# Kernel optimization log

Hardware: AMD Instinct MI355X
Metric: run time of the kernel (lower is better)

## Reference

```python
import jax, jax.numpy as jnp
import numpy as np

B, S, D, H = 2, 4096, 1024, 16
HD = D // H  # 64


def setup_inputs() -> dict:
    key = jax.random.key(0)
    ks = jax.random.split(key, 9)
    init = lambda k, shape: (jax.random.normal(k, shape, dtype=jnp.float32) * 0.02)
    return {
        "x": jax.random.normal(ks[0], (B, S, D), dtype=jnp.float32),
        "Wq": init(ks[1], (D, D)), "bq": init(ks[2], (D,)),
        "Wk": init(ks[3], (D, D)), "bk": init(ks[4], (D,)),
        "Wv": init(ks[5], (D, D)), "bv": init(ks[6], (D,)),
        "Wo": init(ks[7], (D, D)), "bo": init(ks[8], (D,)),
    }


def _split_heads(t):
    # [B, S, D] -> [B, H, S, HD]
    b, s, d = t.shape
    return t.reshape(b, s, H, HD).transpose(0, 2, 1, 3)


def reference(x, Wq, bq, Wk, bk, Wv, bv, Wo, bo):
    # q/k/v projections (torch Linear: x @ W.T + b)
    q = _split_heads(x @ Wq.T + bq)
    k = _split_heads(x @ Wk.T + bk)
    v = _split_heads(x @ Wv.T + bv)
    scale = 1.0 / np.sqrt(HD).astype(np.float32)
    # chunked_attention uses full K/V per chunk => equivalent to full attention.
    scores = jnp.einsum("bhqd,bhkd->bhqk", q, k) * scale
    # softmax computed in fp32 then cast back (matches F.softmax(dtype=float32))
    attn = jax.nn.softmax(scores.astype(jnp.float32), axis=-1).astype(scores.dtype)
    out = jnp.einsum("bhqk,bhkd->bhqd", attn, v)
    out = out.transpose(0, 2, 1, 3).reshape(B, S, D)  # combine heads
    return out @ Wo.T + bo
```

## Files before the change

### kernel.cpp

```cpp
#include <hip/hip_runtime.h>
#include <hip/hip_bf16.h>
#include <stdint.h>

typedef __attribute__((ext_vector_type(8))) short short8;
typedef __attribute__((ext_vector_type(4))) short short4v;
typedef __attribute__((ext_vector_type(4))) float f32x4;
typedef __attribute__((ext_vector_type(4))) unsigned int uint4v;

#define MFMA16(A, B, C) __builtin_amdgcn_mfma_f32_16x16x32_bf16(A, B, C, 0, 0, 0)

#define GLDS16(gp, lp) __builtin_amdgcn_global_load_lds(                     \
    (const __attribute__((address_space(1))) unsigned int*)(gp),             \
    (__attribute__((address_space(3))) unsigned int*)(lp), 16, 0, 0)

static constexpr int kS  = 4096;
static constexpr int kD  = 1024;
static constexpr int kH  = 16;
static constexpr int kHD = 64;

__device__ __forceinline__ short bf16_bits(float f) {
    __hip_bfloat16 h = __float2bfloat16(f);
    return *(short*)&h;
}

__device__ __forceinline__ unsigned int pk_bf16(float a, float b) {
    __hip_bfloat162 h = __float22bfloat162_rn(make_float2(a, b));
    return *(unsigned int*)&h;
}

__device__ __forceinline__ short8 cvt8(const float* __restrict__ p) {
    f32x4 a = ((const f32x4*)p)[0];
    f32x4 b = ((const f32x4*)p)[1];
    short8 r;
    r[0] = bf16_bits(a[0]); r[1] = bf16_bits(a[1]);
    r[2] = bf16_bits(a[2]); r[3] = bf16_bits(a[3]);
    r[4] = bf16_bits(b[0]); r[5] = bf16_bits(b[1]);
    r[6] = bf16_bits(b[2]); r[7] = bf16_bits(b[3]);
    return r;
}

__device__ __forceinline__ unsigned char f32_to_e4m3(float f) {
    unsigned int u = __float_as_uint(f);
    unsigned int s = (u >> 24) & 0x80u;
    unsigned int a = u & 0x7fffffffu;
    if (a < 0x3c800000u) {
        float af = __uint_as_float(a);
        unsigned int sub = (unsigned int)(af * 512.0f + 0.5f);
        return (unsigned char)(s | sub);
    }
    unsigned int r = a + 0x80000u;
    unsigned int m = (r >> 20) & 7u;
    int eb = (int)(r >> 23) - 127 + 7;
    unsigned int bits = ((unsigned int)eb << 3) | m;
    if (bits > 0x7Eu) bits = 0x7Eu;
    return (unsigned char)(s | bits);
}
__device__ __forceinline__ float e4m3_to_f32(unsigned int b) {
    unsigned int s = b & 0x80u;
    unsigned int e = (b >> 3) & 15u;
    unsigned int m = b & 7u;
    float f = e ? __uint_as_float(((e + 120u) << 23) | (m << 20))
                : (float)m * 0.001953125f;
    return s ? -f : f;
}

__global__ __launch_bounds__(256) void cvt_f32_bf16(
    const float* __restrict__ src, __hip_bfloat16* __restrict__ dst)
{
    const int i = blockIdx.x * 256 + threadIdx.x;
    f32x4 v = ((const f32x4*)src)[i];
    short4v o;
    o[0] = bf16_bits(v[0]); o[1] = bf16_bits(v[1]);
    o[2] = bf16_bits(v[2]); o[3] = bf16_bits(v[3]);
    ((short4v*)dst)[i] = o;
}

__global__ __launch_bounds__(256) void cvt_w4(
    const float* __restrict__ w0, const float* __restrict__ w1,
    const float* __restrict__ w2, const float* __restrict__ w3,
    __hip_bfloat16* __restrict__ dst)
{
    const int blk = blockIdx.x;
    const int sel = blk >> 10;
    const float* src = sel == 0 ? w0 : sel == 1 ? w1 : sel == 2 ? w2 : w3;
    const int i = (blk & 1023) * 256 + threadIdx.x;
    f32x4 v = ((const f32x4*)src)[i];
    short4v o;
    o[0] = bf16_bits(v[0]); o[1] = bf16_bits(v[1]);
    o[2] = bf16_bits(v[2]); o[3] = bf16_bits(v[3]);
    ((short4v*)(dst + (size_t)sel * kD * kD))[i] = o;
}


__global__ __launch_bounds__(256) void gemm_qkv(
    const __hip_bfloat16* __restrict__ X, const __hip_bfloat16* __restrict__ Wb,
    const float* __restrict__ bq, const float* __restrict__ bk,
    const float* __restrict__ bv,
    __hip_bfloat16* __restrict__ Qw, __hip_bfloat16* __restrict__ Kw,
    __hip_bfloat16* __restrict__ Vtw)
{
    __shared__ short As[128 * 64];
    __shared__ short Bs[128 * 64];

    const int lane = threadIdx.x & 63, wave = threadIdx.x >> 6;
    const int quad = lane >> 4, l16 = lane & 15;
    const int sel = blockIdx.y >> 3;
    const int m0 = blockIdx.x * 128, n0 = (blockIdx.y & 7) * 128;
    const int wm = wave & 1, wn = wave >> 1;

    const float* bias = sel == 0 ? bq : sel == 1 ? bk : bv;
    const short* Xg = (const short*)X + (size_t)m0 * kD;
    const short* Wg = (const short*)Wb + (size_t)sel * kD * kD + (size_t)n0 * kD;

    f32x4 acc[4][4];
    #pragma unroll
    for (int mt = 0; mt < 4; ++mt)
        #pragma unroll
        for (int nt = 0; nt < 4; ++nt) acc[mt][nt] = f32x4{0.f, 0.f, 0.f, 0.f};

    const int srow = lane >> 3;
    const int gch  = (lane & 7) ^ srow;

    for (int k0 = 0; k0 < kD; k0 += 64) {
        __syncthreads();
        #pragma unroll
        for (int i = 0; i < 4; ++i) {
            const int rowbase = wave * 32 + i * 8;
            const int row = rowbase + srow;
            GLDS16(Xg + (size_t)row * kD + k0 + gch * 8, &As[rowbase * 64]);
            GLDS16(Wg + (size_t)row * kD + k0 + gch * 8, &Bs[rowbase * 64]);
        }
        __syncthreads();

        #pragma unroll
        for (int c = 0; c < 2; ++c) {
            short8 af[4], bf[4];
            const int rx = l16 & 7;
            #pragma unroll
            for (int mt = 0; mt < 4; ++mt)
                af[mt] = *(const short8*)&As[(wm * 64 + mt * 16 + l16) * 64
                                             + (((c * 4 + quad) ^ rx) * 8)];
            #pragma unroll
            for (int nt = 0; nt < 4; ++nt)
                bf[nt] = *(const short8*)&Bs[(wn * 64 + nt * 16 + l16) * 64
                                             + (((c * 4 + quad) ^ rx) * 8)];
            #pragma unroll
            for (int mt = 0; mt < 4; ++mt)
                #pragma unroll
                for (int nt = 0; nt < 4; ++nt)
                    acc[mt][nt] = MFMA16(af[mt], bf[nt], acc[mt][nt]);
        }
    }

    #pragma unroll
    for (int nt = 0; nt < 4; ++nt) {
        const int n = n0 + wn * 64 + nt * 16 + l16;
        const float bvv = bias[n];
        #pragma unroll
        for (int mt = 0; mt < 4; ++mt) {
            if (sel == 2) {
                const int m = m0 + wm * 64 + mt * 16 + quad * 4;
                short4v pk;
                #pragma unroll
                for (int r = 0; r < 4; ++r)
                    pk[r] = bf16_bits(acc[mt][nt][r] + bvv);
                const int bh2 = (m >> 12) * kH + (n >> 6);
                short* dst = (short*)Vtw
                    + ((size_t)bh2 * kHD + (size_t)(n & (kHD - 1))) * kS
                    + (size_t)(m & (kS - 1));
                *(short4v*)dst = pk;
            } else {
                __hip_bfloat16* dst = sel == 0 ? Qw : Kw;
                const float scale = sel == 0 ? 0.18033688f : 1.0f;
                #pragma unroll
                for (int r = 0; r < 4; ++r) {
                    const int m = m0 + wm * 64 + mt * 16 + quad * 4 + r;
                    const float v = (acc[mt][nt][r] + bvv) * scale;
                    const size_t addr = (((size_t)(m >> 12) * kH + (n >> 6)) * kS
                                         + (size_t)(m & (kS - 1))) * kHD
                                        + (size_t)(n & (kHD - 1));
                    dst[addr] = __float2bfloat16(v);
                }
            }
        }
    }
}

__global__ __launch_bounds__(256) void gemm_out(
    const __hip_bfloat16* __restrict__ X, const __hip_bfloat16* __restrict__ W,
    const float* __restrict__ bias, float* __restrict__ out)
{
    __shared__ short As[128 * 64];
    __shared__ short Bs[128 * 64];

    const int lane = threadIdx.x & 63, wave = threadIdx.x >> 6;
    const int quad = lane >> 4, l16 = lane & 15;
    const int m0 = blockIdx.x * 128, n0 = blockIdx.y * 128;
    const int wm = wave & 1, wn = wave >> 1;

    const short* Xg = (const short*)X + (size_t)m0 * kD;
    const short* Wg = (const short*)W + (size_t)n0 * kD;

    f32x4 acc[4][4];
    #pragma unroll
    for (int mt = 0; mt < 4; ++mt)
        #pragma unroll
        for (int nt = 0; nt < 4; ++nt) acc[mt][nt] = f32x4{0.f, 0.f, 0.f, 0.f};

    const int srow = lane >> 3;
    const int gch  = (lane & 7) ^ srow;

    for (int k0 = 0; k0 < kD; k0 += 64) {
        __syncthreads();
        #pragma unroll
        for (int i = 0; i < 4; ++i) {
            const int rowbase = wave * 32 + i * 8;
            const int row = rowbase + srow;
            GLDS16(Xg + (size_t)row * kD + k0 + gch * 8, &As[rowbase * 64]);
            GLDS16(Wg + (size_t)row * kD + k0 + gch * 8, &Bs[rowbase * 64]);
        }
        __syncthreads();

        #pragma unroll
        for (int c = 0; c < 2; ++c) {
            short8 af[4], bf[4];
            const int rx = l16 & 7;
            #pragma unroll
            for (int mt = 0; mt < 4; ++mt)
                af[mt] = *(const short8*)&As[(wm * 64 + mt * 16 + l16) * 64
                                             + (((c * 4 + quad) ^ rx) * 8)];
            #pragma unroll
            for (int nt = 0; nt < 4; ++nt)
                bf[nt] = *(const short8*)&Bs[(wn * 64 + nt * 16 + l16) * 64
                                             + (((c * 4 + quad) ^ rx) * 8)];
            #pragma unroll
            for (int mt = 0; mt < 4; ++mt)
                #pragma unroll
                for (int nt = 0; nt < 4; ++nt)
                    acc[mt][nt] = MFMA16(af[mt], bf[nt], acc[mt][nt]);
        }
    }

    #pragma unroll
    for (int nt = 0; nt < 4; ++nt) {
        const int n = n0 + wn * 64 + nt * 16 + l16;
        const float bv = bias[n];
        #pragma unroll
        for (int mt = 0; mt < 4; ++mt)
            #pragma unroll
            for (int r = 0; r < 4; ++r) {
                const int m = m0 + wm * 64 + mt * 16 + quad * 4 + r;
                out[(size_t)m * kD + n] = acc[mt][nt][r] + bv;
            }
    }
}

__global__ __launch_bounds__(256, 4) void flash2(
    const __hip_bfloat16* __restrict__ Qw, const __hip_bfloat16* __restrict__ Kw,
    const __hip_bfloat16* __restrict__ Vt, __hip_bfloat16* __restrict__ O)
{
    __shared__ short Ks[2][8 * 512];
    __shared__ short Vs[2][8 * 512];

    const int lane = threadIdx.x & 63, wave = threadIdx.x >> 6;
    const int quad = lane >> 4, l16 = lane & 15;

    const int flat = blockIdx.y * 32 + blockIdx.x;
    const int swz  = (flat & 7) * 128 + (flat >> 3);
    const int bh = swz >> 5, b = bh >> 4, h = bh & 15;
    const int qbase = (swz & 31) * 128 + wave * 32;

    const short* Qg = (const short*)Qw + ((size_t)bh * kS + qbase) * kHD;
    short8 qf[2][2];
    #pragma unroll
    for (int t = 0; t < 2; ++t)
        #pragma unroll
        for (int c = 0; c < 2; ++c)
            qf[t][c] = *(const short8*)(Qg + (t * 16 + l16) * kHD + c * 32 + quad * 8);

    const short* Kg = (const short*)Kw + (size_t)bh * kS * kHD;
    const short* Vg = (const short*)Vt + (size_t)bh * kHD * kS;

    const short ONE = 0x3F80;
    const short8 onesf = {ONE, ONE, ONE, ONE, ONE, ONE, ONE, ONE};

    f32x4 o[2][4], lsumv[2];
    #pragma unroll
    for (int t = 0; t < 2; ++t) {
        lsumv[t] = f32x4{0.f, 0.f, 0.f, 0.f};
        #pragma unroll
        for (int dt = 0; dt < 4; ++dt) o[t][dt] = f32x4{0.f, 0.f, 0.f, 0.f};
    }

    const int kc = wave >> 1, km = wave & 1;
    const int krow = kc * 32 + 8 * (l16 >> 2) + 4 * km + (l16 & 3);
    const short* ka0 = Kg + (size_t)krow * kHD + quad * 8;
    const short* ka1 = ka0 + 32;
    const int vdt = (wave & 1) * 2, vc32 = (wave >> 1) * 32;
    const short* va0 = Vg + (size_t)((vdt + 0) * 16 + l16) * kS + vc32 + quad * 8;
    const short* va1 = Vg + (size_t)((vdt + 1) * 16 + l16) * kS + vc32 + quad * 8;

    GLDS16(ka0, &Ks[0][(wave * 2 + 0) * 512]);
    GLDS16(ka1, &Ks[0][(wave * 2 + 1) * 512]);
    GLDS16(va0, &Vs[0][(wave * 2 + 0) * 512]);
    GLDS16(va1, &Vs[0][(wave * 2 + 1) * 512]);
    ka0 += 64 * kHD; ka1 += 64 * kHD; va0 += 64; va1 += 64;

    for (int k0 = 0; k0 < kS; k0 += 64) {
        const int cur = (k0 >> 6) & 1;
        __syncthreads();
        if (k0 + 64 < kS) {
            const int nxt = cur ^ 1;
            GLDS16(ka0, &Ks[nxt][(wave * 2 + 0) * 512]);
            GLDS16(ka1, &Ks[nxt][(wave * 2 + 1) * 512]);
            GLDS16(va0, &Vs[nxt][(wave * 2 + 0) * 512]);
            GLDS16(va1, &Vs[nxt][(wave * 2 + 1) * 512]);
            ka0 += 64 * kHD; ka1 += 64 * kHD; va0 += 64; va1 += 64;
        }

        #pragma unroll
        for (int c = 0; c < 2; ++c) {
            short8 vb[4];
            #pragma unroll
            for (int dt = 0; dt < 4; ++dt)
                vb[dt] = *(const short8*)&Vs[cur][(c * 4 + dt) * 512 + lane * 8];

            unsigned int P[2][4];
            #pragma unroll
            for (int m = 0; m < 2; ++m) {
                const int fb = c * 4 + m * 2;
                short8 a0 = *(const short8*)&Ks[cur][(fb + 0) * 512 + lane * 8];
                short8 a1 = *(const short8*)&Ks[cur][(fb + 1) * 512 + lane * 8];
                #pragma unroll
                for (int t = 0; t < 2; ++t) {
                    f32x4 z = {0.f, 0.f, 0.f, 0.f};
                    f32x4 s = MFMA16(a0, qf[t][0], z);
                    s = MFMA16(a1, qf[t][1], s);
                    P[t][m * 2 + 0] = pk_bf16(__builtin_amdgcn_exp2f(s[0]),
                                              __builtin_amdgcn_exp2f(s[1]));
                    P[t][m * 2 + 1] = pk_bf16(__builtin_amdgcn_exp2f(s[2]),
                                              __builtin_amdgcn_exp2f(s[3]));
                }
            }

            short8 pa[2];
            #pragma unroll
            for (int t = 0; t < 2; ++t) {
                uint4v u = {P[t][0], P[t][1], P[t][2], P[t][3]};
                pa[t] = __builtin_bit_cast(short8, u);
            }

            __builtin_amdgcn_s_setprio(1);
            #pragma unroll
            for (int t = 0; t < 2; ++t)
                lsumv[t] = MFMA16(pa[t], onesf, lsumv[t]);
            #pragma unroll
            for (int dt = 0; dt < 4; ++dt) {
                o[0][dt] = MFMA16(pa[0], vb[dt], o[0][dt]);
                o[1][dt] = MFMA16(pa[1], vb[dt], o[1][dt]);
            }
            __builtin_amdgcn_s_setprio(0);
        }
    }

    #pragma unroll
    for (int t = 0; t < 2; ++t)
        #pragma unroll
        for (int r = 0; r < 4; ++r) {
            const float inv = 1.0f / lsumv[t][r];
            const int sq = qbase + t * 16 + quad * 4 + r;
            #pragma unroll
            for (int dt = 0; dt < 4; ++dt)
                O[((size_t)b * kS + sq) * kD + h * kHD + dt * 16 + l16] =
                    __float2bfloat16(o[t][dt][r] * inv);
        }
}

template <bool KV8, bool WB16>
__global__ __launch_bounds__(256) void gemm_kv(
    const float* __restrict__ X, const void* __restrict__ W,
    const float* __restrict__ bias, void* __restrict__ outv)
{
    const int lane = threadIdx.x & 63;
    const int wave = threadIdx.x >> 6;
    const int quad = lane >> 4;
    const int l16  = lane & 15;
    const int m0 = blockIdx.x * 16;
    const int n0 = blockIdx.y * 256 + wave * 64;

    const float* xr = X + (size_t)(m0 + l16) * kD;
    const float* wf = (const float*)W + (size_t)(n0 + l16) * kD;
    const short* wb = (const short*)W + (size_t)(n0 + l16) * kD;

    f32x4 acc[4] = {{0.f,0.f,0.f,0.f},{0.f,0.f,0.f,0.f},
                    {0.f,0.f,0.f,0.f},{0.f,0.f,0.f,0.f}};

    for (int k8 = quad; k8 < kD / 8; k8 += 4) {
        short8 a = cvt8(xr + k8 * 8);
        #pragma unroll
        for (int nt = 0; nt < 4; ++nt) {
            short8 w = WB16 ? *(const short8*)(wb + nt * 16 * kD + k8 * 8)
                            : cvt8(wf + nt * 16 * kD + k8 * 8);
            acc[nt] = MFMA16(a, w, acc[nt]);
        }
    }

    #pragma unroll
    for (int nt = 0; nt < 4; ++nt) {
        const int n = n0 + nt * 16 + l16;
        const float bv = bias[n];
        #pragma unroll
        for (int r = 0; r < 4; ++r) {
            const int m = m0 + quad * 4 + r;
            const float v = acc[nt][r] + bv;
            const size_t addr = (((size_t)(m >> 12) * kH + (n >> 6)) * kS
                                 + (size_t)(m & (kS - 1))) * kHD + (size_t)(n & (kHD - 1));
            if (KV8) ((unsigned char*)outv)[addr] = f32_to_e4m3(v);
            else     ((__hip_bfloat16*)outv)[addr] = __float2bfloat16(v);
        }
    }
}

template <bool KV8, bool WB16>
__global__ __launch_bounds__(256) void flash_fusedq(
    const float* __restrict__ x,  const void* __restrict__ Wq,
    const float* __restrict__ bq, const void* __restrict__ Kw,
    const void* __restrict__ Vw,  __hip_bfloat16* __restrict__ O)
{
    __shared__ short pool[9216];
    __shared__ short Ps[4][32][72];

    const int lane = threadIdx.x & 63;
    const int wave = threadIdx.x >> 6;
    const int quad = lane >> 4;
    const int l16  = lane & 15;
    const int bh   = blockIdx.y;
    const int b    = bh >> 4, h = bh & 15;
    const int qbase = blockIdx.x * 128 + wave * 32;

    {
        const float* xr0 = x + (size_t)(b * kS + qbase + l16) * kD;
        const float* xr1 = xr0 + (size_t)16 * kD;
        const float* wqf = (const float*)Wq + (size_t)(h * kHD + l16) * kD;
        const short* wqb = (const short*)Wq + (size_t)(h * kHD + l16) * kD;
        f32x4 qa[2][4];
        #pragma unroll
        for (int t = 0; t < 2; ++t)
            #pragma unroll
            for (int nt = 0; nt < 4; ++nt) qa[t][nt] = f32x4{0.f,0.f,0.f,0.f};

        for (int k8 = quad; k8 < kD / 8; k8 += 4) {
            short8 a0 = cvt8(xr0 + k8 * 8);
            short8 a1 = cvt8(xr1 + k8 * 8);
            #pragma unroll
            for (int nt = 0; nt < 4; ++nt) {
                short8 w = WB16 ? *(const short8*)(wqb + nt * 16 * kD + k8 * 8)
                                : cvt8(wqf + nt * 16 * kD + k8 * 8);
                qa[0][nt] = MFMA16(a0, w, qa[0][nt]);
                qa[1][nt] = MFMA16(a1, w, qa[1][nt]);
            }
        }
        #pragma unroll
        for (int t = 0; t < 2; ++t)
            #pragma unroll
            for (int nt = 0; nt < 4; ++nt) {
                const float bv = bq[h * kHD + nt * 16 + l16];
                #pragma unroll
                for (int r = 0; r < 4; ++r)
                    pool[wave * 2304 + (t * 16 + quad * 4 + r) * 72 + nt * 16 + l16] =
                        bf16_bits((qa[t][nt][r] + bv) * 0.125f);
            }
    }
    short8 qf[2][2];
    #pragma unroll
    for (int t = 0; t < 2; ++t)
        #pragma unroll
        for (int c = 0; c < 2; ++c)
            qf[t][c] = *(const short8*)&pool[wave * 2304 + (t * 16 + l16) * 72 + c * 32 + quad * 8];

    f32x4 o[2][4];
    float mrow[2][4], lrow[2][4];
    #pragma unroll
    for (int t = 0; t < 2; ++t)
        #pragma unroll
        for (int dt = 0; dt < 4; ++dt) o[t][dt] = f32x4{0.f,0.f,0.f,0.f};
    #pragma unroll
    for (int t = 0; t < 2; ++t)
        #pragma unroll
        for (int r = 0; r < 4; ++r) { mrow[t][r] = -INFINITY; lrow[t][r] = 0.f; }

    const __hip_bfloat16* Kb16 = (const __hip_bfloat16*)Kw + (size_t)bh * kS * kHD;
    const __hip_bfloat16* Vb16 = (const __hip_bfloat16*)Vw + (size_t)bh * kS * kHD;
    const unsigned char*  K8   = (const unsigned char*)Kw + (size_t)bh * kS * kHD;
    const unsigned char*  V8   = (const unsigned char*)Vw + (size_t)bh * kS * kHD;

    for (int k0 = 0; k0 < kS; k0 += 64) {
        __syncthreads();
        #pragma unroll
        for (int i = 0; i < 2; ++i) {
            const int lin = threadIdx.x + i * 256;
            const int kr = lin >> 3, c8 = lin & 7;
            short8 kv, vv;
            if (KV8) {
                uint2 kbits = *(const uint2*)(K8 + (size_t)(k0 + kr) * kHD + c8 * 8);
                uint2 vbits = *(const uint2*)(V8 + (size_t)(k0 + kr) * kHD + c8 * 8);
                #pragma unroll
                for (int j = 0; j < 4; ++j) {
                    kv[j]     = bf16_bits(e4m3_to_f32((kbits.x >> (8 * j)) & 255u));
                    kv[4 + j] = bf16_bits(e4m3_to_f32((kbits.y >> (8 * j)) & 255u));
                    vv[j]     = bf16_bits(e4m3_to_f32((vbits.x >> (8 * j)) & 255u));
                    vv[4 + j] = bf16_bits(e4m3_to_f32((vbits.y >> (8 * j)) & 255u));
                }
            } else {
                kv = *(const short8*)(Kb16 + (size_t)(k0 + kr) * kHD + c8 * 8);
                vv = *(const short8*)(Vb16 + (size_t)(k0 + kr) * kHD + c8 * 8);
            }
            *(short8*)&pool[kr * 72 + c8 * 8] = kv;
            #pragma unroll
            for (int j = 0; j < 8; ++j)
                pool[4608 + (c8 * 8 + j) * 72 + (((kr >> 3) ^ c8) << 3) + (kr & 7)] = vv[j];
        }
        __syncthreads();

        f32x4 sc[2][4];
        #pragma unroll
        for (int kt = 0; kt < 4; ++kt) {
            short8 b0 = *(const short8*)&pool[(kt * 16 + l16) * 72 + quad * 8];
            short8 b1 = *(const short8*)&pool[(kt * 16 + l16) * 72 + 32 + quad * 8];
            f32x4 z = {0.f, 0.f, 0.f, 0.f};
            f32x4 s0 = MFMA16(qf[0][0], b0, z); s0 = MFMA16(qf[0][1], b1, s0);
            f32x4 s1 = MFMA16(qf[1][0], b0, z); s1 = MFMA16(qf[1][1], b1, s1);
            sc[0][kt] = s0; sc[1][kt] = s1;
        }

        #pragma unroll
        for (int t = 0; t < 2; ++t)
            #pragma unroll
            for (int r = 0; r < 4; ++r) {
                float s0 = sc[t][0][r], s1 = sc[t][1][r];
                float s2 = sc[t][2][r], s3 = sc[t][3][r];
                float mx = fmaxf(fmaxf(s0, s1), fmaxf(s2, s3));
                #pragma unroll
                for (int off = 1; off < 16; off <<= 1)
                    mx = fmaxf(mx, __shfl_xor(mx, off, 64));
                const float mnew  = fmaxf(mrow[t][r], mx);
                const float alpha = __builtin_amdgcn_exp2f((mrow[t][r] - mnew) * 1.44269504f);
                mrow[t][r] = mnew;
                const float p0 = __builtin_amdgcn_exp2f((s0 - mnew) * 1.44269504f);
                const float p1 = __builtin_amdgcn_exp2f((s1 - mnew) * 1.44269504f);
                const float p2 = __builtin_amdgcn_exp2f((s2 - mnew) * 1.44269504f);
                const float p3 = __builtin_amdgcn_exp2f((s3 - mnew) * 1.44269504f);
                float ps = (p0 + p1) + (p2 + p3);
                #pragma unroll
                for (int off = 1; off < 16; off <<= 1)
                    ps += __shfl_xor(ps, off, 64);
                lrow[t][r] = lrow[t][r] * alpha + ps;
                o[t][0][r] *= alpha; o[t][1][r] *= alpha;
                o[t][2][r] *= alpha; o[t][3][r] *= alpha;
                const int row = t * 16 + quad * 4 + r;
                Ps[wave][row][l16]      = bf16_bits(p0);
                Ps[wave][row][16 + l16] = bf16_bits(p1);
                Ps[wave][row][32 + l16] = bf16_bits(p2);
                Ps[wave][row][48 + l16] = bf16_bits(p3);
            }

        short8 pa[2][2];
        #pragma unroll
        for (int t = 0; t < 2; ++t)
            #pragma unroll
            for (int c = 0; c < 2; ++c)
                pa[t][c] = *(const short8*)&Ps[wave][t * 16 + l16][c * 32 + quad * 8];
        #pragma unroll
        for (int c = 0; c < 2; ++c)
            #pragma unroll
            for (int dt = 0; dt < 4; ++dt) {
                const int d = dt * 16 + l16;
                short8 vb = *(const short8*)&pool[4608 + d * 72 + ((((c * 4 + quad)) ^ (d >> 3)) << 3)];
                o[0][dt] = MFMA16(pa[0][c], vb, o[0][dt]);
                o[1][dt] = MFMA16(pa[1][c], vb, o[1][dt]);
            }
    }

    #pragma unroll
    for (int t = 0; t < 2; ++t)
        #pragma unroll
        for (int r = 0; r < 4; ++r) {
            const float inv = 1.0f / lrow[t][r];
            const int sq = qbase + t * 16 + quad * 4 + r;
            #pragma unroll
            for (int dt = 0; dt < 4; ++dt)
                O[((size_t)b * kS + sq) * kD + h * kHD + dt * 16 + l16] =
                    __float2bfloat16(o[t][dt][r] * inv);
        }
}

template <bool WB16>
__global__ __launch_bounds__(256) void proj_out(
    const __hip_bfloat16* __restrict__ Xb, const void* __restrict__ W,
    const float* __restrict__ bias, float* __restrict__ out)
{
    const int lane = threadIdx.x & 63;
    const int wave = threadIdx.x >> 6;
    const int quad = lane >> 4;
    const int l16  = lane & 15;
    const int m0 = blockIdx.x * 16;
    const int n0 = blockIdx.y * 256 + wave * 64;

    const short8* xr = (const short8*)((const short*)Xb + (size_t)(m0 + l16) * kD);
    const float*  wf = (const float*)W + (size_t)(n0 + l16) * kD;
    const short*  wb = (const short*)W + (size_t)(n0 + l16) * kD;

    f32x4 acc[4] = {{0.f,0.f,0.f,0.f},{0.f,0.f,0.f,0.f},
                    {0.f,0.f,0.f,0.f},{0.f,0.f,0.f,0.f}};

    for (int k8 = quad; k8 < kD / 8; k8 += 4) {
        short8 a = xr[k8];
        #pragma unroll
        for (int nt = 0; nt < 4; ++nt) {
            short8 w = WB16 ? *(const short8*)(wb + nt * 16 * kD + k8 * 8)
                            : cvt8(wf + nt * 16 * kD + k8 * 8);
            acc[nt] = MFMA16(a, w, acc[nt]);
        }
    }

    #pragma unroll
    for (int nt = 0; nt < 4; ++nt) {
        const int n = n0 + nt * 16 + l16;
        const float bv = bias[n];
        #pragma unroll
        for (int r = 0; r < 4; ++r) {
            const int m = m0 + quad * 4 + r;
            out[(size_t)m * kD + n] = acc[nt][r] + bv;
        }
    }
}

extern "C" void kernel_launch(void* const* d_in, const int* in_sizes, int n_in,
                              void* d_out, int out_size, void* d_ws, size_t ws_size,
                              hipStream_t stream)
{
    const float* x = nullptr;
    const float* Wm[4] = {nullptr, nullptr, nullptr, nullptr};
    const float* bm[4] = {nullptr, nullptr, nullptr, nullptr};
    int wi = 0, bi = 0;
    for (int i = 0; i < n_in; ++i) {
        const int s = in_sizes[i];
        if      (s == 2 * kS * kD)         x = (const float*)d_in[i];
        else if (s == kD * kD && wi < 4)   Wm[wi++] = (const float*)d_in[i];
        else if (s == kD      && bi < 4)   bm[bi++] = (const float*)d_in[i];
    }
    const float *Wq = Wm[0], *Wk = Wm[1], *Wv = Wm[2], *Wo = Wm[3];
    const float *bq = bm[0], *bk = bm[1], *bv = bm[2], *bo = bm[3];
    float* out = (float*)d_out;

    const size_t elems = (size_t)2 * kS * kD;
    const size_t wel   = (size_t)kD * kD;
    const size_t MB = 1024 * 1024;
    dim3 bb(256);

    if (ws_size >= 88 * MB) {
        __hip_bfloat16* xb  = (__hip_bfloat16*)d_ws;
        __hip_bfloat16* Qw  = xb + elems;
        __hip_bfloat16* Kw  = Qw + elems;
        __hip_bfloat16* Vtw = Kw + elems;
        __hip_bfloat16* Ow  = Vtw + elems;
        __hip_bfloat16* Wqb = Ow + elems;
        __hip_bfloat16* Wob = Wqb + 3 * wel;

        cvt_f32_bf16<<<dim3(8192), bb, 0, stream>>>(x, xb);
        cvt_w4<<<dim3(4096), bb, 0, stream>>>(Wq, Wk, Wv, Wo, Wqb);

        gemm_qkv<<<dim3(64, 24), bb, 0, stream>>>(xb, Wqb, bq, bk, bv, Qw, Kw, Vtw);
        flash2<<<dim3(kS / 128, 32), bb, 0, stream>>>(Qw, Kw, Vtw, Ow);
        gemm_out<<<dim3(64, 8), bb, 0, stream>>>(Ow, Wob, bo, out);
        return;
    }

    dim3 gg(512, 4), gf(kS / 128, 2 * kH);
    if (ws_size >= 56 * MB) {
        __hip_bfloat16* Kw  = (__hip_bfloat16*)d_ws;
        __hip_bfloat16* Vw  = Kw + elems;
        __hip_bfloat16* Ow  = Vw + elems;
        __hip_bfloat16* Wqb = Ow + elems;
        __hip_bfloat16* Wkb = Wqb + wel;
        __hip_bfloat16* Wvb = Wkb + wel;
        __hip_bfloat16* Wob = Wvb + wel;
        cvt_w4<<<dim3(4096), bb, 0, stream>>>(Wq, Wk, Wv, Wo, Wqb);
        gemm_kv<false, true><<<gg, bb, 0, stream>>>(x, Wkb, bk, Kw);
        gemm_kv<false, true><<<gg, bb, 0, stream>>>(x, Wvb, bv, Vw);
        flash_fusedq<false, true><<<gf, bb, 0, stream>>>(x, Wqb, bq, Kw, Vw, Ow);
        proj_out<true><<<gg, bb, 0, stream>>>(Ow, Wob, bo, out);
    } else if (ws_size >= 48 * MB) {
        __hip_bfloat16* Kw = (__hip_bfloat16*)d_ws;
        __hip_bfloat16* Vw = Kw + elems;
        __hip_bfloat16* Ow = Vw + elems;
        gemm_kv<false, false><<<gg, bb, 0, stream>>>(x, Wk, bk, Kw);
        gemm_kv<false, false><<<gg, bb, 0, stream>>>(x, Wv, bv, Vw);
        flash_fusedq<false, false><<<gf, bb, 0, stream>>>(x, Wq, bq, Kw, Vw, Ow);
        proj_out<false><<<gg, bb, 0, stream>>>(Ow, Wo, bo, out);
    } else {
        unsigned char* Kw = (unsigned char*)d_ws;
        unsigned char* Vw = Kw + elems;
        __hip_bfloat16* Ow = (__hip_bfloat16*)(Vw + elems);
        gemm_kv<true, false><<<gg, bb, 0, stream>>>(x, Wk, bk, Kw);
        gemm_kv<true, false><<<gg, bb, 0, stream>>>(x, Wv, bv, Vw);
        flash_fusedq<true, false><<<gf, bb, 0, stream>>>(x, Wq, bq, Kw, Vw, Ow);
        proj_out<false><<<gg, bb, 0, stream>>>(Ow, Wo, bo, out);
    }
}
```

Measured before the change: 344.1 us.

## Deepen flash attention K/V pipeline to four 32-key stages with explicit vmcnt waits

The flash attention loop now stages K/V in four 32-key buffers instead of two 64-key buffers, keeping three loads in flight. Each phase waits on vmcnt for only the oldest load and uses a raw s_barrier instead of __syncthreads, so global-to-LDS loads overlap more with MFMA work. The loop is unrolled by four with a hand-written drain at the end. This adds barriers per key (one per 32 keys), and the vmcnt accounting is fragile if the compiler reorders other memory operations.

```diff
diff --git a/kernel.cpp b/kernel.cpp
--- a/kernel.cpp
+++ b/kernel.cpp
@@ -259,8 +259,8 @@
     const __hip_bfloat16* __restrict__ Qw, const __hip_bfloat16* __restrict__ Kw,
     const __hip_bfloat16* __restrict__ Vt, __hip_bfloat16* __restrict__ O)
 {
-    __shared__ short Ks[2][8 * 512];
-    __shared__ short Vs[2][8 * 512];
+    __shared__ short Ks[4][4 * 512];
+    __shared__ short Vs[4][4 * 512];
 
     const int lane = threadIdx.x & 63, wave = threadIdx.x >> 6;
     const int quad = lane >> 4, l16 = lane & 15;
@@ -277,6 +277,12 @@
         #pragma unroll
         for (int c = 0; c < 2; ++c)
             qf[t][c] = *(const short8*)(Qg + (t * 16 + l16) * kHD + c * 32 + quad * 8);
+    #pragma unroll
+    for (int t = 0; t < 2; ++t)
+        #pragma unroll
+        for (int c = 0; c < 2; ++c)
+            asm volatile("" : "+v"(qf[t][c]));
+    asm volatile("s_waitcnt vmcnt(0)" ::: "memory");
 
     const short* Kg = (const short*)Kw + (size_t)bh * kS * kHD;
     const short* Vg = (const short*)Vt + (size_t)bh * kHD * kS;
@@ -292,76 +298,75 @@
         for (int dt = 0; dt < 4; ++dt) o[t][dt] = f32x4{0.f, 0.f, 0.f, 0.f};
     }
 
-    const int kc = wave >> 1, km = wave & 1;
-    const int krow = kc * 32 + 8 * (l16 >> 2) + 4 * km + (l16 & 3);
-    const short* ka0 = Kg + (size_t)krow * kHD + quad * 8;
-    const short* ka1 = ka0 + 32;
-    const int vdt = (wave & 1) * 2, vc32 = (wave >> 1) * 32;
-    const short* va0 = Vg + (size_t)((vdt + 0) * 16 + l16) * kS + vc32 + quad * 8;
-    const short* va1 = Vg + (size_t)((vdt + 1) * 16 + l16) * kS + vc32 + quad * 8;
-
-    GLDS16(ka0, &Ks[0][(wave * 2 + 0) * 512]);
-    GLDS16(ka1, &Ks[0][(wave * 2 + 1) * 512]);
-    GLDS16(va0, &Vs[0][(wave * 2 + 0) * 512]);
-    GLDS16(va1, &Vs[0][(wave * 2 + 1) * 512]);
-    ka0 += 64 * kHD; ka1 += 64 * kHD; va0 += 64; va1 += 64;
-
-    for (int k0 = 0; k0 < kS; k0 += 64) {
-        const int cur = (k0 >> 6) & 1;
-        __syncthreads();
-        if (k0 + 64 < kS) {
-            const int nxt = cur ^ 1;
-            GLDS16(ka0, &Ks[nxt][(wave * 2 + 0) * 512]);
-            GLDS16(ka1, &Ks[nxt][(wave * 2 + 1) * 512]);
-            GLDS16(va0, &Vs[nxt][(wave * 2 + 0) * 512]);
-            GLDS16(va1, &Vs[nxt][(wave * 2 + 1) * 512]);
-            ka0 += 64 * kHD; ka1 += 64 * kHD; va0 += 64; va1 += 64;
-        }
-
-        #pragma unroll
-        for (int c = 0; c < 2; ++c) {
-            short8 vb[4];
-            #pragma unroll
-            for (int dt = 0; dt < 4; ++dt)
-                vb[dt] = *(const short8*)&Vs[cur][(c * 4 + dt) * 512 + lane * 8];
-
-            unsigned int P[2][4];
-            #pragma unroll
-            for (int m = 0; m < 2; ++m) {
-                const int fb = c * 4 + m * 2;
-                short8 a0 = *(const short8*)&Ks[cur][(fb + 0) * 512 + lane * 8];
-                short8 a1 = *(const short8*)&Ks[cur][(fb + 1) * 512 + lane * 8];
-                #pragma unroll
-                for (int t = 0; t < 2; ++t) {
-                    f32x4 z = {0.f, 0.f, 0.f, 0.f};
-                    f32x4 s = MFMA16(a0, qf[t][0], z);
-                    s = MFMA16(a1, qf[t][1], s);
-                    P[t][m * 2 + 0] = pk_bf16(__builtin_amdgcn_exp2f(s[0]),
-                                              __builtin_amdgcn_exp2f(s[1]));
-                    P[t][m * 2 + 1] = pk_bf16(__builtin_amdgcn_exp2f(s[2]),
-                                              __builtin_amdgcn_exp2f(s[3]));
-                }
-            }
-
-            short8 pa[2];
-            #pragma unroll
-            for (int t = 0; t < 2; ++t) {
-                uint4v u = {P[t][0], P[t][1], P[t][2], P[t][3]};
-                pa[t] = __builtin_bit_cast(short8, u);
-            }
-
-            __builtin_amdgcn_s_setprio(1);
-            #pragma unroll
-            for (int t = 0; t < 2; ++t)
-                lsumv[t] = MFMA16(pa[t], onesf, lsumv[t]);
-            #pragma unroll
-            for (int dt = 0; dt < 4; ++dt) {
-                o[0][dt] = MFMA16(pa[0], vb[dt], o[0][dt]);
-                o[1][dt] = MFMA16(pa[1], vb[dt], o[1][dt]);
-            }
-            __builtin_amdgcn_s_setprio(0);
-        }
-    }
+    const int kfidx = 2 * (wave & 1) + (wave >> 1);
+    const short* ka = Kg + (size_t)(8 * (l16 >> 2) + 4 * (wave & 1) + (l16 & 3)) * kHD
+                    + (wave >> 1) * 32 + quad * 8;
+    const short* va = Vg + (size_t)(wave * 16 + l16) * kS + quad * 8;
+
+    #pragma unroll
+    for (int p = 0; p < 3; ++p) {
+        GLDS16(ka, &Ks[p][kfidx * 512]);  ka += 32 * kHD;
+        GLDS16(va, &Vs[p][wave * 512]);   va += 32;
+    }
+
+    #define PHASE(BUF, IBUF, VM, DO_ISSUE)                                     \
+    {                                                                          \
+        asm volatile("s_waitcnt vmcnt(" #VM ")" ::: "memory");                 \
+        __builtin_amdgcn_s_barrier();                                          \
+        __builtin_amdgcn_sched_barrier(0);                                     \
+        if (DO_ISSUE) {                                                        \
+            GLDS16(ka, &Ks[IBUF][kfidx * 512]);  ka += 32 * kHD;               \
+            GLDS16(va, &Vs[IBUF][wave * 512]);   va += 32;                     \
+        }                                                                      \
+        short8 vb[4];                                                          \
+        _Pragma("unroll")                                                      \
+        for (int dt = 0; dt < 4; ++dt)                                         \
+            vb[dt] = *(const short8*)&Vs[BUF][dt * 512 + lane * 8];            \
+        unsigned int P[2][4];                                                  \
+        _Pragma("unroll")                                                      \
+        for (int m = 0; m < 2; ++m) {                                          \
+            short8 a0 = *(const short8*)&Ks[BUF][(m * 2 + 0) * 512 + lane * 8];\
+            short8 a1 = *(const short8*)&Ks[BUF][(m * 2 + 1) * 512 + lane * 8];\
+            _Pragma("unroll")                                                  \
+            for (int t = 0; t < 2; ++t) {                                      \
+                f32x4 z = {0.f, 0.f, 0.f, 0.f};                                \
+                f32x4 s = MFMA16(a0, qf[t][0], z);                             \
+                s = MFMA16(a1, qf[t][1], s);                                   \
+                P[t][m * 2 + 0] = pk_bf16(__builtin_amdgcn_exp2f(s[0]),        \
+                                          __builtin_amdgcn_exp2f(s[1]));       \
+                P[t][m * 2 + 1] = pk_bf16(__builtin_amdgcn_exp2f(s[2]),        \
+                                          __builtin_amdgcn_exp2f(s[3]));       \
+            }                                                                  \
+        }                                                                      \
+        short8 pa[2];                                                          \
+        _Pragma("unroll")                                                      \
+        for (int t = 0; t < 2; ++t) {                                          \
+            uint4v u = {P[t][0], P[t][1], P[t][2], P[t][3]};                   \
+            pa[t] = __builtin_bit_cast(short8, u);                             \
+        }                                                                      \
+        __builtin_amdgcn_s_setprio(1);                                         \
+        _Pragma("unroll")                                                      \
+        for (int t = 0; t < 2; ++t)                                            \
+            lsumv[t] = MFMA16(pa[t], onesf, lsumv[t]);                         \
+        _Pragma("unroll")                                                      \
+        for (int dt = 0; dt < 4; ++dt) {                                       \
+            o[0][dt] = MFMA16(pa[0], vb[dt], o[0][dt]);                        \
+            o[1][dt] = MFMA16(pa[1], vb[dt], o[1][dt]);                        \
+        }                                                                      \
+        __builtin_amdgcn_s_setprio(0);                                         \
+    }
+
+    for (int h0 = 0; h0 < 124; h0 += 4) {
+        PHASE(0, 3, 4, true)
+        PHASE(1, 0, 4, true)
+        PHASE(2, 1, 4, true)
+        PHASE(3, 2, 4, true)
+    }
+    PHASE(0, 3, 4, true)
+    PHASE(1, 0, 4, false)
+    PHASE(2, 0, 2, false)
+    PHASE(3, 0, 0, false)
+    #undef PHASE
 
     #pragma unroll
     for (int t = 0; t < 2; ++t)
```

Result: slower. 364.4 us (+5.9%).

## Double flash attention query tile per wave and fuse conversion kernels

Applied to the files above, without the earlier changes.

The flash attention kernel now handles 64 query rows per wave (256 per block) instead of 32, so each K/V tile loaded into LDS is reused across twice as many queries. The grid is halved to match, and the launch bound drops to 2 blocks per CU to make room for the larger accumulator register footprint. Separately, the x and weight fp32-to-bf16 conversions are merged into one launch to save a kernel launch. The risks are lower occupancy and fewer blocks than needed to fill all CUs (512 blocks).

```diff
diff --git a/kernel.cpp b/kernel.cpp
--- a/kernel.cpp
+++ b/kernel.cpp
@@ -89,6 +89,32 @@
     o[0] = bf16_bits(v[0]); o[1] = bf16_bits(v[1]);
     o[2] = bf16_bits(v[2]); o[3] = bf16_bits(v[3]);
     ((short4v*)(dst + (size_t)sel * kD * kD))[i] = o;
+}
+
+__global__ __launch_bounds__(256) void cvt_all(
+    const float* __restrict__ x,
+    const float* __restrict__ w0, const float* __restrict__ w1,
+    const float* __restrict__ w2, const float* __restrict__ w3,
+    __hip_bfloat16* __restrict__ xb, __hip_bfloat16* __restrict__ wdst)
+{
+    int blk = blockIdx.x;
+    const float* src;
+    __hip_bfloat16* dst;
+    int i;
+    if (blk < 8192) {
+        src = x; dst = xb; i = blk * 256 + threadIdx.x;
+    } else {
+        blk -= 8192;
+        const int sel = blk >> 10;
+        src = sel == 0 ? w0 : sel == 1 ? w1 : sel == 2 ? w2 : w3;
+        dst = wdst + (size_t)sel * kD * kD;
+        i = (blk & 1023) * 256 + threadIdx.x;
+    }
+    f32x4 v = ((const f32x4*)src)[i];
+    short4v o;
+    o[0] = bf16_bits(v[0]); o[1] = bf16_bits(v[1]);
+    o[2] = bf16_bits(v[2]); o[3] = bf16_bits(v[3]);
+    ((short4v*)dst)[i] = o;
 }
 
 
@@ -255,7 +281,7 @@
     }
 }
 
-__global__ __launch_bounds__(256, 4) void flash2(
+__global__ __launch_bounds__(256, 2) void flash2(
     const __hip_bfloat16* __restrict__ Qw, const __hip_bfloat16* __restrict__ Kw,
     const __hip_bfloat16* __restrict__ Vt, __hip_bfloat16* __restrict__ O)
 {
@@ -265,15 +291,15 @@
     const int lane = threadIdx.x & 63, wave = threadIdx.x >> 6;
     const int quad = lane >> 4, l16 = lane & 15;
 
-    const int flat = blockIdx.y * 32 + blockIdx.x;
-    const int swz  = (flat & 7) * 128 + (flat >> 3);
-    const int bh = swz >> 5, b = bh >> 4, h = bh & 15;
-    const int qbase = (swz & 31) * 128 + wave * 32;
+    const int flat = blockIdx.y * 16 + blockIdx.x;
+    const int swz  = (flat & 7) * 64 + (flat >> 3);
+    const int bh = swz >> 4, b = bh >> 4, h = bh & 15;
+    const int qbase = (swz & 15) * 256 + wave * 64;
 
     const short* Qg = (const short*)Qw + ((size_t)bh * kS + qbase) * kHD;
-    short8 qf[2][2];
-    #pragma unroll
-    for (int t = 0; t < 2; ++t)
+    short8 qf[4][2];
+    #pragma unroll
+    for (int t = 0; t < 4; ++t)
         #pragma unroll
         for (int c = 0; c < 2; ++c)
             qf[t][c] = *(const short8*)(Qg + (t * 16 + l16) * kHD + c * 32 + quad * 8);
@@ -284,9 +310,9 @@
     const short ONE = 0x3F80;
     const short8 onesf = {ONE, ONE, ONE, ONE, ONE, ONE, ONE, ONE};
 
-    f32x4 o[2][4], lsumv[2];
-    #pragma unroll
-    for (int t = 0; t < 2; ++t) {
+    f32x4 o[4][4], lsumv[4];
+    #pragma unroll
+    for (int t = 0; t < 4; ++t) {
         lsumv[t] = f32x4{0.f, 0.f, 0.f, 0.f};
         #pragma unroll
         for (int dt = 0; dt < 4; ++dt) o[t][dt] = f32x4{0.f, 0.f, 0.f, 0.f};
@@ -325,14 +351,14 @@
             for (int dt = 0; dt < 4; ++dt)
                 vb[dt] = *(const short8*)&Vs[cur][(c * 4 + dt) * 512 + lane * 8];
 
-            unsigned int P[2][4];
+            unsigned int P[4][4];
             #pragma unroll
             for (int m = 0; m < 2; ++m) {
                 const int fb = c * 4 + m * 2;
                 short8 a0 = *(const short8*)&Ks[cur][(fb + 0) * 512 + lane * 8];
                 short8 a1 = *(const short8*)&Ks[cur][(fb + 1) * 512 + lane * 8];
                 #pragma unroll
-                for (int t = 0; t < 2; ++t) {
+                for (int t = 0; t < 4; ++t) {
                     f32x4 z = {0.f, 0.f, 0.f, 0.f};
                     f32x4 s = MFMA16(a0, qf[t][0], z);
                     s = MFMA16(a1, qf[t][1], s);
@@ -343,28 +369,28 @@
                 }
             }
 
-            short8 pa[2];
-            #pragma unroll
-            for (int t = 0; t < 2; ++t) {
+            short8 pa[4];
+            #pragma unroll
+            for (int t = 0; t < 4; ++t) {
                 uint4v u = {P[t][0], P[t][1], P[t][2], P[t][3]};
                 pa[t] = __builtin_bit_cast(short8, u);
             }
 
             __builtin_amdgcn_s_setprio(1);
             #pragma unroll
-            for (int t = 0; t < 2; ++t)
+            for (int t = 0; t < 4; ++t)
                 lsumv[t] = MFMA16(pa[t], onesf, lsumv[t]);
             #pragma unroll
-            for (int dt = 0; dt < 4; ++dt) {
-                o[0][dt] = MFMA16(pa[0], vb[dt], o[0][dt]);
-                o[1][dt] = MFMA16(pa[1], vb[dt], o[1][dt]);
-            }
+            for (int dt = 0; dt < 4; ++dt)
+                #pragma unroll
+                for (int t = 0; t < 4; ++t)
+                    o[t][dt] = MFMA16(pa[t], vb[dt], o[t][dt]);
             __builtin_amdgcn_s_setprio(0);
         }
     }
 
     #pragma unroll
-    for (int t = 0; t < 2; ++t)
+    for (int t = 0; t < 4; ++t)
         #pragma unroll
         for (int r = 0; r < 4; ++r) {
             const float inv = 1.0f / lsumv[t][r];
@@ -667,11 +693,10 @@
         __hip_bfloat16* Wqb = Ow + elems;
         __hip_bfloat16* Wob = Wqb + 3 * wel;
 
-        cvt_f32_bf16<<<dim3(8192), bb, 0, stream>>>(x, xb);
-        cvt_w4<<<dim3(4096), bb, 0, stream>>>(Wq, Wk, Wv, Wo, Wqb);
+        cvt_all<<<dim3(12288), bb, 0, stream>>>(x, Wq, Wk, Wv, Wo, xb, Wqb);
 
         gemm_qkv<<<dim3(64, 24), bb, 0, stream>>>(xb, Wqb, bq, bk, bv, Qw, Kw, Vtw);
-        flash2<<<dim3(kS / 128, 32), bb, 0, stream>>>(Qw, Kw, Vtw, Ow);
+        flash2<<<dim3(16, 32), bb, 0, stream>>>(Qw, Kw, Vtw, Ow);
         gemm_out<<<dim3(64, 8), bb, 0, stream>>>(Ow, Wob, bo, out);
         return;
     }
```

Result: no change. 345.0 us (+0.3%).
